# Performance work log

Hardware: AMD Instinct MI355X
Metric: run time of the kernel (lower is better)

The kernel has to match this reference:

```python
import jax, jax.numpy as jnp
import numpy as np


def setup_inputs() -> dict:
    key = jax.random.key(0)
    k1, k2 = jax.random.split(key)
    x = jax.random.normal(k1, (32, 56, 56, 256), dtype=jnp.float32)
    conv_w = jax.random.normal(k2, (7, 7, 2, 1), dtype=jnp.float32) * 0.1
    conv_b = jnp.zeros((1,), dtype=jnp.float32)
    return {"x": x, "conv_w": conv_w, "conv_b": conv_b}


def reference(x, conv_w, conv_b):
    # x: [B, H, W, C] (NHWC, as in Keras)
    avg_pool = jnp.mean(x, axis=-1, keepdims=True)          # [B,H,W,1]
    max_pool = jnp.max(x, axis=-1, keepdims=True)           # [B,H,W,1]
    concat = jnp.concatenate([avg_pool, max_pool], axis=-1)  # [B,H,W,2]
    # 7x7 'same' conv, 2 -> 1 channels, HWIO kernel layout
    attn = jax.lax.conv_general_dilated(
        concat, conv_w,
        window_strides=(1, 1), padding='SAME',
        dimension_numbers=('NHWC', 'HWIO', 'NHWC'))
    attn = jax.nn.sigmoid(attn + conv_b)                     # [B,H,W,1]
    return x * attn
```

## Files before the change

kernel.cpp:

```cpp
#include <hip/hip_runtime.h>
#include <math.h>

#define BB 32
#define HH 56
#define WW 56
#define CC 256
#define NPIX (BB * HH * WW)

__global__ __launch_bounds__(256) void pool_kernel(const float* __restrict__ x,
                                                   float* __restrict__ pooled) {
    int pix  = blockIdx.x * 4 + (threadIdx.x >> 6);
    int lane = threadIdx.x & 63;
    const float4* x4 = (const float4*)x;
    float4 v = x4[(size_t)pix * 64 + lane];
    float s = v.x + v.y + v.z + v.w;
    float m = fmaxf(fmaxf(v.x, v.y), fmaxf(v.z, v.w));
#pragma unroll
    for (int o = 32; o > 0; o >>= 1) {
        s += __shfl_down(s, o, 64);
        m = fmaxf(m, __shfl_down(m, o, 64));
    }
    if (lane == 0) {
        pooled[pix * 2]     = s * (1.0f / 256.0f);
        pooled[pix * 2 + 1] = m;
    }
}

__global__ __launch_bounds__(256) void conv_kernel(const float* __restrict__ pooled,
                                                   const float* __restrict__ cw,
                                                   const float* __restrict__ cb,
                                                   float* __restrict__ attn) {
    int idx = blockIdx.x * 256 + threadIdx.x;
    if (idx >= NPIX) return;
    int b  = idx / (HH * WW);
    int hw = idx % (HH * WW);
    int h  = hw / WW;
    int w  = hw % WW;
    float acc = cb[0];
    const float* base = pooled + (size_t)b * HH * WW * 2;
#pragma unroll
    for (int dh = 0; dh < 7; ++dh) {
        int ih = h + dh - 3;
        if (ih < 0 || ih >= HH) continue;
#pragma unroll
        for (int dw = 0; dw < 7; ++dw) {
            int iw = w + dw - 3;
            if (iw < 0 || iw >= WW) continue;
            const float* p = base + (ih * WW + iw) * 2;
            const float* k = cw + (dh * 7 + dw) * 2;
            acc = fmaf(p[0], k[0], acc);
            acc = fmaf(p[1], k[1], acc);
        }
    }
    attn[idx] = 1.0f / (1.0f + expf(-acc));
}

__global__ __launch_bounds__(256) void scale_kernel(const float* __restrict__ x,
                                                    const float* __restrict__ attn,
                                                    float* __restrict__ out) {
    size_t i = (size_t)blockIdx.x * 256 + threadIdx.x;
    const float4* x4 = (const float4*)x;
    float4* o4 = (float4*)out;
    float a = attn[i >> 6];
    float4 v = x4[i];
    v.x *= a; v.y *= a; v.z *= a; v.w *= a;
    o4[i] = v;
}

extern "C" void kernel_launch(void* const* d_in, const int* in_sizes, int n_in,
                              void* d_out, int out_size, void* d_ws, size_t ws_size,
                              hipStream_t stream) {
    const float* x  = (const float*)d_in[0];
    const float* cw = (const float*)d_in[1];
    const float* cb = (const float*)d_in[2];
    float* out = (float*)d_out;

    float* pooled = (float*)d_ws;
    float* attn   = pooled + (size_t)NPIX * 2;

    pool_kernel<<<NPIX / 4, 256, 0, stream>>>(x, pooled);
    conv_kernel<<<(NPIX + 255) / 256, 256, 0, stream>>>(pooled, cw, cb, attn);
    scale_kernel<<<NPIX / 4, 256, 0, stream>>>(x, attn, out);
}
```

Baseline: 200.8 us.

## Fuse conv and scale into one kernel, pool four pixels per wavefront

Merges the 7x7 conv, sigmoid and scaling into one kernel where each wavefront handles one pixel: lanes 0-48 each compute one conv tap, the taps are summed with a wave reduction, and the result scales the pixel's channels. This drops one launch and the write and read of the attention buffer. The pool kernel now processes four pixels per wavefront with independent loads to raise memory-level parallelism, and writes its outputs as float4. The fused kernel does 49 gathered pooled loads and a shuffle reduction per pixel, which adds some latency to a bandwidth-bound pass.

After: 195.4 us. 1.03x faster.

```diff
diff --git a/kernel.cpp b/kernel.cpp
--- a/kernel.cpp
+++ b/kernel.cpp
@@ -9,62 +9,72 @@
 
 __global__ __launch_bounds__(256) void pool_kernel(const float* __restrict__ x,
                                                    float* __restrict__ pooled) {
-    int pix  = blockIdx.x * 4 + (threadIdx.x >> 6);
+    int wid  = blockIdx.x * 4 + (threadIdx.x >> 6);
     int lane = threadIdx.x & 63;
     const float4* x4 = (const float4*)x;
-    float4 v = x4[(size_t)pix * 64 + lane];
-    float s = v.x + v.y + v.z + v.w;
-    float m = fmaxf(fmaxf(v.x, v.y), fmaxf(v.z, v.w));
+    size_t base = ((size_t)wid << 8) | (size_t)lane;
+
+    float s[4], m[4];
+#pragma unroll
+    for (int i = 0; i < 4; ++i) {
+        float4 v = x4[base + (size_t)i * 64];
+        s[i] = (v.x + v.y) + (v.z + v.w);
+        m[i] = fmaxf(fmaxf(v.x, v.y), fmaxf(v.z, v.w));
+    }
 #pragma unroll
     for (int o = 32; o > 0; o >>= 1) {
-        s += __shfl_down(s, o, 64);
-        m = fmaxf(m, __shfl_down(m, o, 64));
+#pragma unroll
+        for (int i = 0; i < 4; ++i) {
+            s[i] += __shfl_down(s[i], o, 64);
+            m[i] = fmaxf(m[i], __shfl_down(m[i], o, 64));
+        }
     }
     if (lane == 0) {
-        pooled[pix * 2]     = s * (1.0f / 256.0f);
-        pooled[pix * 2 + 1] = m;
+        float4* p4 = (float4*)pooled;
+        p4[wid * 2]     = make_float4(s[0] * (1.0f / 256.0f), m[0],
+                                      s[1] * (1.0f / 256.0f), m[1]);
+        p4[wid * 2 + 1] = make_float4(s[2] * (1.0f / 256.0f), m[2],
+                                      s[3] * (1.0f / 256.0f), m[3]);
     }
 }
 
-__global__ __launch_bounds__(256) void conv_kernel(const float* __restrict__ pooled,
-                                                   const float* __restrict__ cw,
-                                                   const float* __restrict__ cb,
-                                                   float* __restrict__ attn) {
-    int idx = blockIdx.x * 256 + threadIdx.x;
-    if (idx >= NPIX) return;
-    int b  = idx / (HH * WW);
-    int hw = idx % (HH * WW);
+__global__ __launch_bounds__(256) void fused_kernel(const float* __restrict__ x,
+                                                    const float* __restrict__ pooled,
+                                                    const float* __restrict__ cw,
+                                                    const float* __restrict__ cb,
+                                                    float* __restrict__ out) {
+    int pix  = blockIdx.x * 4 + (threadIdx.x >> 6);
+    int lane = threadIdx.x & 63;
+
+    size_t xi = ((size_t)pix << 6) | (size_t)lane;
+    const float4* x4 = (const float4*)x;
+    float4 v = x4[xi];
+
+    int b  = pix / (HH * WW);
+    int hw = pix % (HH * WW);
     int h  = hw / WW;
     int w  = hw % WW;
-    float acc = cb[0];
-    const float* base = pooled + (size_t)b * HH * WW * 2;
-#pragma unroll
-    for (int dh = 0; dh < 7; ++dh) {
+
+    float acc = 0.0f;
+    if (lane < 49) {
+        int dh = lane / 7;
+        int dw = lane - dh * 7;
         int ih = h + dh - 3;
-        if (ih < 0 || ih >= HH) continue;
-#pragma unroll
-        for (int dw = 0; dw < 7; ++dw) {
-            int iw = w + dw - 3;
-            if (iw < 0 || iw >= WW) continue;
-            const float* p = base + (ih * WW + iw) * 2;
-            const float* k = cw + (dh * 7 + dw) * 2;
-            acc = fmaf(p[0], k[0], acc);
-            acc = fmaf(p[1], k[1], acc);
+        int iw = w + dw - 3;
+        if (ih >= 0 && ih < HH && iw >= 0 && iw < WW) {
+            const float2* p2 = (const float2*)pooled;
+            float2 p = p2[(b * HH + ih) * WW + iw];
+            float2 k = ((const float2*)cw)[lane];
+            acc = fmaf(p.y, k.y, p.x * k.x);
         }
     }
-    attn[idx] = 1.0f / (1.0f + expf(-acc));
-}
+#pragma unroll
+    for (int o = 32; o > 0; o >>= 1) acc += __shfl_down(acc, o, 64);
+    float a = __shfl(acc, 0, 64) + cb[0];
+    a = 1.0f / (1.0f + expf(-a));
 
-__global__ __launch_bounds__(256) void scale_kernel(const float* __restrict__ x,
-                                                    const float* __restrict__ attn,
-                                                    float* __restrict__ out) {
-    size_t i = (size_t)blockIdx.x * 256 + threadIdx.x;
-    const float4* x4 = (const float4*)x;
-    float4* o4 = (float4*)out;
-    float a = attn[i >> 6];
-    float4 v = x4[i];
     v.x *= a; v.y *= a; v.z *= a; v.w *= a;
-    o4[i] = v;
+    ((float4*)out)[xi] = v;
 }
 
 extern "C" void kernel_launch(void* const* d_in, const int* in_sizes, int n_in,
@@ -76,9 +86,7 @@
     float* out = (float*)d_out;
 
     float* pooled = (float*)d_ws;
-    float* attn   = pooled + (size_t)NPIX * 2;
 
-    pool_kernel<<<NPIX / 4, 256, 0, stream>>>(x, pooled);
-    conv_kernel<<<(NPIX + 255) / 256, 256, 0, stream>>>(pooled, cw, cb, attn);
-    scale_kernel<<<NPIX / 4, 256, 0, stream>>>(x, attn, out);
+    pool_kernel<<<NPIX / 16, 256, 0, stream>>>(x, pooled);
+    fused_kernel<<<NPIX / 4, 256, 0, stream>>>(x, pooled, cw, cb, out);
 }
```
